# Kernel optimization log

Hardware: AMD Instinct MI355X
Metric: run time of the kernel (lower is better)

The kernel has to match this reference:

```python
import jax, jax.numpy as jnp
import numpy as np

D_MODEL, D_HIDDEN, N_EXPERTS, TOP_K = 1024, 2048, 8, 2


def setup_inputs() -> dict:
    key = jax.random.key(0)
    ks = jax.random.split(key, 8)
    s_in = 1.0 / np.sqrt(D_MODEL)
    s_hid = 1.0 / np.sqrt(D_HIDDEN)
    return {
        "x": jax.random.normal(ks[0], (1, 2048, D_MODEL), dtype=jnp.float32),
        # stacked expert weights, stored (in, out) so y = x @ W + b
        "W1": jax.random.normal(ks[1], (N_EXPERTS, D_MODEL, D_HIDDEN), dtype=jnp.float32) * s_in,
        "b1": jnp.zeros((N_EXPERTS, D_HIDDEN), dtype=jnp.float32),
        "W2": jax.random.normal(ks[2], (N_EXPERTS, D_MODEL, D_HIDDEN), dtype=jnp.float32) * s_in,
        "b2": jnp.zeros((N_EXPERTS, D_HIDDEN), dtype=jnp.float32),
        "Wo": jax.random.normal(ks[3], (N_EXPERTS, D_HIDDEN, D_MODEL), dtype=jnp.float32) * s_hid,
        "bo": jnp.zeros((N_EXPERTS, D_MODEL), dtype=jnp.float32),
        "Wr": jax.random.normal(ks[4], (D_MODEL, N_EXPERTS), dtype=jnp.float32) * s_in,
        "br": jnp.zeros((N_EXPERTS,), dtype=jnp.float32),
    }


def reference(x, W1, b1, W2, b2, Wo, bo, Wr, br):
    B, S, D = x.shape
    T = B * S
    xf = x.reshape(T, D)

    # router
    logits = xf @ Wr + br                      # [T, E]
    probs = jax.nn.softmax(logits, axis=-1)
    topk_probs, topk_idx = jax.lax.top_k(probs, TOP_K)  # [T, K]

    # combine weights: c[t, e] = sum_k topk_probs[t, k] * 1[topk_idx[t, k] == e]
    c = jnp.zeros((T, N_EXPERTS), dtype=xf.dtype)
    c = c.at[jnp.arange(T)[:, None], topk_idx].add(topk_probs)  # [T, E]

    # per-expert SwiGLU FFN applied densely, then masked-combined (same math
    # as the original gather/scatter loop since c[t,e]=0 for unrouted experts)
    h = jnp.einsum('td,edh->eth', xf, W1) + b1[:, None, :]   # [E, T, H]
    g = jnp.einsum('td,edh->eth', xf, W2) + b2[:, None, :]
    y = jnp.einsum('eth,ehd->etd', h * jax.nn.silu(g), Wo) + bo[:, None, :]
    out = jnp.einsum('etd,te->td', y, c).reshape(B, S, D)

    probs_mean = probs.mean(axis=0)
    lb_loss = (probs_mean * probs_mean).sum() * N_EXPERTS
    return out, lb_loss
```

## Files before the change

### kernel.cpp

```cpp
#include <hip/hip_runtime.h>
#include <hip/hip_bf16.h>

#define T_TOK 2048
#define DM 1024
#define DH 2048
#define NE 8
#define MT_MAX 40

using bf16x8 = __attribute__((ext_vector_type(8))) short;
using f32x4  = __attribute__((ext_vector_type(4))) float;

__device__ __forceinline__ unsigned short f2bf(float f) {
  union { float f; unsigned u; } v; v.f = f;
  unsigned r = v.u + 0x7FFFu + ((v.u >> 16) & 1u);
  return (unsigned short)(r >> 16);
}
__device__ __forceinline__ unsigned pk2(float a, float b) {
  return (unsigned)f2bf(a) | ((unsigned)f2bf(b) << 16);
}

#define GLOAD16(gsrc, ldst)                                                        \
  __builtin_amdgcn_global_load_lds(                                                \
      (const __attribute__((address_space(1))) unsigned int*)(gsrc),               \
      (__attribute__((address_space(3))) unsigned int*)(ldst), 16, 0, 0)

__global__ void k_init(int* __restrict__ cnt) {
  if (threadIdx.x < NE) cnt[threadIdx.x] = 0;
}

__global__ __launch_bounds__(256) void k_wconv(
    const float* __restrict__ x, const float* __restrict__ Wr, const float* __restrict__ br,
    int* __restrict__ cnt, int* __restrict__ idx, float* __restrict__ wgt,
    int* __restrict__ t2r, float* __restrict__ probs, unsigned short* __restrict__ xb,
    const float* __restrict__ W1, const float* __restrict__ W2, const float* __restrict__ Wo,
    unsigned short* __restrict__ W1T, unsigned short* __restrict__ W2T,
    unsigned short* __restrict__ WoT)
{
  __shared__ __align__(16) unsigned short tb[2][64*64];
  const int tid = threadIdx.x;

  if (blockIdx.x < 512) {
    const int wave = tid >> 6, l = tid & 63;
    const int tok = blockIdx.x * 4 + wave;
    float xv[16];
#pragma unroll
    for (int i = 0; i < 16; ++i) xv[i] = x[tok*DM + l + 64*i];
#pragma unroll
    for (int i = 0; i < 16; ++i) xb[tok*DM + l + 64*i] = f2bf(xv[i]);

    float acc[8] = {0.f,0.f,0.f,0.f,0.f,0.f,0.f,0.f};
#pragma unroll
    for (int i = 0; i < 16; ++i) {
      const float4* wp = (const float4*)&Wr[(size_t)(l + 64*i)*NE];
      float4 wa = wp[0], wb = wp[1];
      acc[0] += xv[i]*wa.x; acc[1] += xv[i]*wa.y; acc[2] += xv[i]*wa.z; acc[3] += xv[i]*wa.w;
      acc[4] += xv[i]*wb.x; acc[5] += xv[i]*wb.y; acc[6] += xv[i]*wb.z; acc[7] += xv[i]*wb.w;
    }
#pragma unroll
    for (int e = 0; e < 8; ++e) {
#pragma unroll
      for (int off = 32; off; off >>= 1) acc[e] += __shfl_xor(acc[e], off, 64);
      acc[e] += br[e];
    }
    float mx = acc[0];
#pragma unroll
    for (int e = 1; e < 8; ++e) mx = fmaxf(mx, acc[e]);
    float p[8], s = 0.f;
#pragma unroll
    for (int e = 0; e < 8; ++e) { p[e] = expf(acc[e] - mx); s += p[e]; }
    float inv = 1.f / s;
#pragma unroll
    for (int e = 0; e < 8; ++e) p[e] *= inv;

    int e0 = 0; float p0 = p[0];
#pragma unroll
    for (int e = 1; e < 8; ++e) if (p[e] > p0) { p0 = p[e]; e0 = e; }
    int e1 = -1; float p1 = -1.f;
#pragma unroll
    for (int e = 0; e < 8; ++e) { if (e == e0) continue; if (p[e] > p1) { p1 = p[e]; e1 = e; } }

    if (l == 0) {
#pragma unroll
      for (int e = 0; e < 8; ++e) probs[tok*NE + e] = p[e];
      int pos0 = atomicAdd(&cnt[e0], 1);
      idx[e0*T_TOK + pos0] = tok; wgt[e0*T_TOK + pos0] = p0;
      t2r[tok*2 + 0] = e0*T_TOK + pos0;
      int pos1 = atomicAdd(&cnt[e1], 1);
      idx[e1*T_TOK + pos1] = tok; wgt[e1*T_TOK + pos1] = p1;
      t2r[tok*2 + 1] = e1*T_TOK + pos1;
    }
    return;
  }

  const int bx = tid >> 4;
  const int by = tid & 15;
  const int rn = tid >> 3;
  const int sl8 = tid & 7;

#pragma unroll
  for (int it = 0; it < 4; ++it) {
    int tt = (blockIdx.x - 512) * 4 + it;
    const float* in; unsigned short* outT; int nCs;
    int R, C;
    if (tt < 4096)      { in = W1; outT = W1T; R = DM; C = DH; nCs = 5; }
    else if (tt < 8192) { in = W2; outT = W2T; R = DM; C = DH; nCs = 5; tt -= 4096; }
    else                { in = Wo; outT = WoT; R = DH; C = DM; nCs = 4; tt -= 8192; }
    const int e  = tt >> 9;
    const int te = tt & 511;
    const int r0 = (te >> nCs) << 6;
    const int c0 = (te & ((1 << nCs) - 1)) << 6;

    float4 v[4];
#pragma unroll
    for (int i = 0; i < 4; ++i)
      v[i] = *(const float4*)&in[((size_t)e*R + r0 + bx*4 + i)*C + c0 + by*4];

    unsigned short* B = tb[it & 1];
#pragma unroll
    for (int j = 0; j < 4; ++j) {
      int n = by*4 + j;
      uint2 w;
      w.x = pk2(((const float*)&v[0])[j], ((const float*)&v[1])[j]);
      w.y = pk2(((const float*)&v[2])[j], ((const float*)&v[3])[j]);
      int byteoff = n*128 + (((bx >> 1) ^ ((n >> 2) & 7)) * 16) + (bx & 1) * 8;
      *(uint2*)((char*)B + byteoff) = w;
    }
    __syncthreads();

#pragma unroll
    for (int h = 0; h < 2; ++h) {
      int n = rn + h*32;
      int byteoff = n*128 + ((sl8 ^ ((n >> 2) & 7)) * 16);
      uint4 w = *(const uint4*)((const char*)B + byteoff);
      *(uint4*)&outT[((size_t)e*C + c0 + n)*R + r0 + sl8*8] = w;
    }
  }
}

__global__ __launch_bounds__(256) void k_finalize(
    const int* __restrict__ cnt, int* __restrict__ rb,
    const float* __restrict__ probs, float* __restrict__ out,
    int* __restrict__ MTp, int* __restrict__ mtab)
{
  __shared__ float red[8][256];
  const int tid = threadIdx.x;
  float s[8] = {0.f,0.f,0.f,0.f,0.f,0.f,0.f,0.f};
  for (int t = tid; t < T_TOK; t += 256) {
#pragma unroll
    for (int e = 0; e < 8; ++e) s[e] += probs[t*NE + e];
  }
#pragma unroll
  for (int e = 0; e < 8; ++e) red[e][tid] = s[e];
  __syncthreads();
  for (int w = 128; w > 0; w >>= 1) {
    if (tid < w) {
#pragma unroll
      for (int e = 0; e < 8; ++e) red[e][tid] += red[e][tid + w];
    }
    __syncthreads();
  }
  if (tid == 0) {
    float lb = 0.f;
#pragma unroll
    for (int e = 0; e < 8; ++e) {
      float mean = red[e][0] * (1.f / T_TOK);
      lb += mean * mean;
    }
    out[2097152] = lb * NE;
    int r = 0, mc = 0;
#pragma unroll
    for (int e = 0; e < 8; ++e) {
      rb[e] = r; r += cnt[e];
      int nmt = (cnt[e] + 127) / 128;
      for (int j = 0; j < nmt; ++j) mtab[mc++] = (e << 16) | j;
    }
    *MTp = mc;
  }
}

#define TM1 128
#define TN1 64
#define BKK 64

__global__ __launch_bounds__(256) void k_ffn1b(
    const unsigned short* __restrict__ xb,
    const unsigned short* __restrict__ W1T, const float* __restrict__ b1,
    const unsigned short* __restrict__ W2T, const float* __restrict__ b2,
    const int* __restrict__ cnt, const int* __restrict__ rbp,
    const int* __restrict__ idx, unsigned short* __restrict__ act,
    const int* __restrict__ MTp, const int* __restrict__ mtab)
{
  const int mtg = blockIdx.y;
  if (mtg >= *MTp) return;
  const int code = mtab[mtg];
  const int e = code >> 16, mt = code & 0xffff;
  const int Me = cnt[e];
  const int m0 = mt * TM1;
  const int nt = blockIdx.x;
  const int n0 = nt * TN1;

  __shared__ __align__(16) unsigned short As[TM1*BKK];
  __shared__ __align__(16) unsigned short Bh[TN1*BKK];
  __shared__ __align__(16) unsigned short Bg[TN1*BKK];
  __shared__ int toks[TM1];

  const int tid = threadIdx.x;
  if (tid < TM1) toks[tid] = idx[e*T_TOK + min(m0 + tid, Me - 1)];
  __syncthreads();

  const int lane = tid & 63;
  const int wave = tid >> 6;
  const int wm = wave >> 1, wn = wave & 1;
  const int row16 = lane & 15, kg = lane >> 4;
  const int sl = lane & 7;
  const int lr = lane >> 3;

  const unsigned short* asrc[4];
#pragma unroll
  for (int i = 0; i < 4; ++i) {
    int r = (wave*4 + i)*8 + lr;
    asrc[i] = &xb[(size_t)toks[r]*DM + ((sl ^ (r & 7)) * 8)];
  }
  const unsigned short *bsrc1[2], *bsrc2[2];
#pragma unroll
  for (int j = 0; j < 2; ++j) {
    int r = (wave*2 + j)*8 + lr;
    size_t gb = ((size_t)e*DH + n0 + r)*DM + ((sl ^ (r & 7)) * 8);
    bsrc1[j] = &W1T[gb]; bsrc2[j] = &W2T[gb];
  }

  f32x4 ah[4][2], ag[4][2];
#pragma unroll
  for (int i = 0; i < 4; ++i)
#pragma unroll
    for (int j = 0; j < 2; ++j) { ah[i][j] = 0.f; ag[i][j] = 0.f; }

  for (int k0 = 0; k0 < DM; k0 += BKK) {
#pragma unroll
    for (int i = 0; i < 4; ++i)
      GLOAD16(asrc[i] + k0, &As[(wave*4 + i)*512]);
#pragma unroll
    for (int j = 0; j < 2; ++j) {
      GLOAD16(bsrc1[j] + k0, &Bh[(wave*2 + j)*512]);
      GLOAD16(bsrc2[j] + k0, &Bg[(wave*2 + j)*512]);
    }
    __syncthreads();
#pragma unroll
    for (int ks = 0; ks < 2; ++ks) {
      const int kslot = ks*4 + kg;
      bf16x8 a[4], vbh[2], vbg[2];
#pragma unroll
      for (int mi = 0; mi < 4; ++mi) {
        int m = wm*64 + mi*16 + row16;
        a[mi] = *(const bf16x8*)&As[m*BKK + ((kslot ^ (m & 7)) * 8)];
      }
#pragma unroll
      for (int ni = 0; ni < 2; ++ni) {
        int n = wn*32 + ni*16 + row16;
        int off = n*BKK + ((kslot ^ (n & 7)) * 8);
        vbh[ni] = *(const bf16x8*)&Bh[off];
        vbg[ni] = *(const bf16x8*)&Bg[off];
      }
#pragma unroll
      for (int mi = 0; mi < 4; ++mi)
#pragma unroll
        for (int ni = 0; ni < 2; ++ni) {
          ah[mi][ni] = __builtin_amdgcn_mfma_f32_16x16x32_bf16(a[mi], vbh[ni], ah[mi][ni], 0, 0, 0);
          ag[mi][ni] = __builtin_amdgcn_mfma_f32_16x16x32_bf16(a[mi], vbg[ni], ag[mi][ni], 0, 0, 0);
        }
    }
    __syncthreads();
  }

  const int rb = rbp[e];
#pragma unroll
  for (int mi = 0; mi < 4; ++mi) {
#pragma unroll
    for (int i = 0; i < 4; ++i) {
      int rloc = wm*64 + mi*16 + (lane >> 4)*4 + i;
      int m = m0 + rloc;
      if (m < Me) {
#pragma unroll
        for (int ni = 0; ni < 2; ++ni) {
          int col = n0 + wn*32 + ni*16 + row16;
          float h = ah[mi][ni][i] + b1[e*DH + col];
          float g = ag[mi][ni][i] + b2[e*DH + col];
          float sg = g / (1.f + __expf(-g));
          act[(size_t)(rb + m)*DH + col] = f2bf(h * sg);
        }
      }
    }
  }
}

__global__ __launch_bounds__(256) void k_ffn2b(
    const unsigned short* __restrict__ act,
    const unsigned short* __restrict__ WoT, const float* __restrict__ bo,
    const int* __restrict__ cnt, const int* __restrict__ rbp,
    float* __restrict__ ys,
    const int* __restrict__ MTp, const int* __restrict__ mtab)
{
  const int mtg = blockIdx.y;
  if (mtg >= *MTp) return;
  const int code = mtab[mtg];
  const int e = code >> 16, mt = code & 0xffff;
  const int Me = cnt[e];
  const int m0 = mt * TM1;
  const int nt = blockIdx.x;
  const int n0 = nt * TN1;
  const int rb = rbp[e];

  __shared__ __align__(16) unsigned short As[TM1*BKK];
  __shared__ __align__(16) unsigned short Bs[TN1*BKK];

  const int tid = threadIdx.x;
  const int lane = tid & 63;
  const int wave = tid >> 6;
  const int wm = wave >> 1, wn = wave & 1;
  const int row16 = lane & 15, kg = lane >> 4;
  const int sl = lane & 7;
  const int lr = lane >> 3;

  const unsigned short* asrc[4];
#pragma unroll
  for (int i = 0; i < 4; ++i) {
    int r = (wave*4 + i)*8 + lr;
    int grow = rb + min(m0 + r, Me - 1);
    asrc[i] = &act[(size_t)grow*DH + ((sl ^ (r & 7)) * 8)];
  }
  const unsigned short* bsrc[2];
#pragma unroll
  for (int j = 0; j < 2; ++j) {
    int r = (wave*2 + j)*8 + lr;
    bsrc[j] = &WoT[((size_t)e*DM + n0 + r)*DH + ((sl ^ (r & 7)) * 8)];
  }

  f32x4 acc[4][2];
#pragma unroll
  for (int i = 0; i < 4; ++i)
#pragma unroll
    for (int j = 0; j < 2; ++j) acc[i][j] = 0.f;

  for (int k0 = 0; k0 < DH; k0 += BKK) {
#pragma unroll
    for (int i = 0; i < 4; ++i)
      GLOAD16(asrc[i] + k0, &As[(wave*4 + i)*512]);
#pragma unroll
    for (int j = 0; j < 2; ++j)
      GLOAD16(bsrc[j] + k0, &Bs[(wave*2 + j)*512]);
    __syncthreads();
#pragma unroll
    for (int ks = 0; ks < 2; ++ks) {
      const int kslot = ks*4 + kg;
      bf16x8 a[4], b[2];
#pragma unroll
      for (int mi = 0; mi < 4; ++mi) {
        int m = wm*64 + mi*16 + row16;
        a[mi] = *(const bf16x8*)&As[m*BKK + ((kslot ^ (m & 7)) * 8)];
      }
#pragma unroll
      for (int ni = 0; ni < 2; ++ni) {
        int n = wn*32 + ni*16 + row16;
        b[ni] = *(const bf16x8*)&Bs[n*BKK + ((kslot ^ (n & 7)) * 8)];
      }
#pragma unroll
      for (int mi = 0; mi < 4; ++mi)
#pragma unroll
        for (int ni = 0; ni < 2; ++ni)
          acc[mi][ni] = __builtin_amdgcn_mfma_f32_16x16x32_bf16(a[mi], b[ni], acc[mi][ni], 0, 0, 0);
    }
    __syncthreads();
  }

#pragma unroll
  for (int mi = 0; mi < 4; ++mi) {
#pragma unroll
    for (int i = 0; i < 4; ++i) {
      int rloc = wm*64 + mi*16 + (lane >> 4)*4 + i;
      int m = m0 + rloc;
      if (m < Me) {
#pragma unroll
        for (int ni = 0; ni < 2; ++ni) {
          int col = n0 + wn*32 + ni*16 + row16;
          ys[(size_t)(rb + m)*DM + col] = acc[mi][ni][i] + bo[e*DM + col];
        }
      }
    }
  }
}

__global__ __launch_bounds__(256) void k_combine(
    const float* __restrict__ ys, const int* __restrict__ t2r,
    const int* __restrict__ rbp, const float* __restrict__ wgt,
    float* __restrict__ out)
{
  const int t = blockIdx.x, tid = threadIdx.x;
  const int c0 = t2r[t*2 + 0], c1 = t2r[t*2 + 1];
  const float w0 = wgt[c0], w1 = wgt[c1];
  const int r0 = rbp[c0 >> 11] + (c0 & 2047);
  const int r1 = rbp[c1 >> 11] + (c1 & 2047);
  const float4* p0 = (const float4*)&ys[(size_t)r0*DM];
  const float4* p1 = (const float4*)&ys[(size_t)r1*DM];
  float4* po = (float4*)&out[(size_t)t*DM];
  float4 a = p0[tid], b = p1[tid];
  float4 r;
  r.x = w0*a.x + w1*b.x; r.y = w0*a.y + w1*b.y;
  r.z = w0*a.z + w1*b.z; r.w = w0*a.w + w1*b.w;
  po[tid] = r;
}

extern "C" void kernel_launch(void* const* d_in, const int* in_sizes, int n_in,
                              void* d_out, int out_size, void* d_ws, size_t ws_size,
                              hipStream_t stream)
{
  const float* x  = (const float*)d_in[0];
  const float* W1 = (const float*)d_in[1];
  const float* b1 = (const float*)d_in[2];
  const float* W2 = (const float*)d_in[3];
  const float* b2 = (const float*)d_in[4];
  const float* Wo = (const float*)d_in[5];
  const float* bo = (const float*)d_in[6];
  const float* Wr = (const float*)d_in[7];
  const float* br = (const float*)d_in[8];
  float* out = (float*)d_out;

  char* ws = (char*)d_ws;
  int*   cnt   = (int*)(ws + 0);
  int*   rb    = (int*)(ws + 64);
  int*   MTp   = (int*)(ws + 128);
  int*   mtab  = (int*)(ws + 192);
  int*   t2r   = (int*)(ws + 4096);
  int*   idx   = (int*)(ws + 32*1024);
  float* wgt   = (float*)(ws + 96*1024);
  float* probs = (float*)(ws + 160*1024);
  unsigned short* xb  = (unsigned short*)(ws + 256*1024);
  unsigned short* act = (unsigned short*)(ws + 5ull*1024*1024);
  float* ysb = (float*)(ws + 21ull*1024*1024);
  unsigned short* W1T = (unsigned short*)(ws + 40ull*1024*1024);
  unsigned short* W2T = (unsigned short*)(ws + 72ull*1024*1024);
  unsigned short* WoT = (unsigned short*)(ws + 104ull*1024*1024);

  k_init<<<1, 64, 0, stream>>>(cnt);
  k_wconv<<<512 + 3072, 256, 0, stream>>>(x, Wr, br, cnt, idx, wgt, t2r, probs, xb,
                                          W1, W2, Wo, W1T, W2T, WoT);
  k_finalize<<<1, 256, 0, stream>>>(cnt, rb, probs, out, MTp, mtab);
  k_ffn1b<<<dim3(DH/TN1, MT_MAX), 256, 0, stream>>>(xb, W1T, b1, W2T, b2, cnt, rb, idx, act, MTp, mtab);
  k_ffn2b<<<dim3(DM/TN1, MT_MAX), 256, 0, stream>>>(act, WoT, bo, cnt, rb, ysb, MTp, mtab);
  k_combine<<<T_TOK, 256, 0, stream>>>(ysb, t2r, rb, wgt, out);
}
```

Baseline: 219.4 us.

## Store transposed bf16 weights in contiguous 256x64 tiles for streaming writes

The weight conversion kernel now has each block handle one 64-row by 256-column tile in a single pass. It writes the bf16 result as a contiguous 32KB chunk, replacing the strided transposed rows. The GEMM kernels change their B-operand addressing to read this tiled layout, stepping through K-chunks with a fixed stride. The aim is fully coalesced, sequential stores in the conversion, which happens inside the timed region, and more contiguous weight reads in the GEMMs. In exchange the block uses a larger LDS buffer, and the chunk pointer line contains an odd comma expression that happens to evaluate correctly.

```diff
diff --git a/kernel.cpp b/kernel.cpp
--- a/kernel.cpp
+++ b/kernel.cpp
@@ -36,7 +36,7 @@
     unsigned short* __restrict__ W1T, unsigned short* __restrict__ W2T,
     unsigned short* __restrict__ WoT)
 {
-  __shared__ __align__(16) unsigned short tb[2][64*64];
+  __shared__ __align__(16) unsigned short tb[256*64];
   const int tid = threadIdx.x;
 
   if (blockIdx.x < 512) {
@@ -92,48 +92,46 @@
     return;
   }
 
-  const int bx = tid >> 4;
-  const int by = tid & 15;
-  const int rn = tid >> 3;
-  const int sl8 = tid & 7;
-
-#pragma unroll
-  for (int it = 0; it < 4; ++it) {
-    int tt = (blockIdx.x - 512) * 4 + it;
-    const float* in; unsigned short* outT; int nCs;
-    int R, C;
-    if (tt < 4096)      { in = W1; outT = W1T; R = DM; C = DH; nCs = 5; }
-    else if (tt < 8192) { in = W2; outT = W2T; R = DM; C = DH; nCs = 5; tt -= 4096; }
-    else                { in = Wo; outT = WoT; R = DH; C = DM; nCs = 4; tt -= 8192; }
-    const int e  = tt >> 9;
-    const int te = tt & 511;
-    const int r0 = (te >> nCs) << 6;
-    const int c0 = (te & ((1 << nCs) - 1)) << 6;
-
+  int tt = blockIdx.x - 512;
+  const float* in; unsigned short* outT; int R, C, nTb;
+  if (tt < 1024)      { in = W1; outT = W1T; R = DM; C = DH; nTb = 3; }
+  else if (tt < 2048) { in = W2; outT = W2T; R = DM; C = DH; nTb = 3; tt -= 1024; }
+  else                { in = Wo; outT = WoT; R = DH; C = DM; nTb = 2; tt -= 2048; }
+  const int e  = tt >> 7;
+  const int te = tt & 127;
+  const int r0 = (te >> nTb) * 64;
+  const int c0 = (te & ((1 << nTb) - 1)) * 256;
+
+  const int nq = tid & 63;
+  const int kqb = tid >> 6;
+
+#pragma unroll
+  for (int p = 0; p < 4; ++p) {
+    const int kq = p*4 + kqb;
     float4 v[4];
 #pragma unroll
     for (int i = 0; i < 4; ++i)
-      v[i] = *(const float4*)&in[((size_t)e*R + r0 + bx*4 + i)*C + c0 + by*4];
-
-    unsigned short* B = tb[it & 1];
+      v[i] = *(const float4*)&in[((size_t)e*R + r0 + kq*4 + i)*C + c0 + nq*4];
 #pragma unroll
     for (int j = 0; j < 4; ++j) {
-      int n = by*4 + j;
+      const int n = nq*4 + j;
       uint2 w;
       w.x = pk2(((const float*)&v[0])[j], ((const float*)&v[1])[j]);
       w.y = pk2(((const float*)&v[2])[j], ((const float*)&v[3])[j]);
-      int byteoff = n*128 + (((bx >> 1) ^ ((n >> 2) & 7)) * 16) + (bx & 1) * 8;
-      *(uint2*)((char*)B + byteoff) = w;
-    }
-    __syncthreads();
-
-#pragma unroll
-    for (int h = 0; h < 2; ++h) {
-      int n = rn + h*32;
-      int byteoff = n*128 + ((sl8 ^ ((n >> 2) & 7)) * 16);
-      uint4 w = *(const uint4*)((const char*)B + byteoff);
-      *(uint4*)&outT[((size_t)e*C + c0 + n)*R + r0 + sl8*8] = w;
-    }
+      const int slot8 = kq ^ ((nq & 7) << 1);
+      *(uint2*)((char*)tb + n*128 + slot8*8) = w;
+    }
+  }
+  __syncthreads();
+
+  unsigned short* chunk = outT + (size_t)(blockIdx.x >= 2560 + 512 - 3072 + 3072 ? 0 : 0, (size_t)( ( (e << 7) | te ) ) * 16384);
+#pragma unroll
+  for (int p2 = 0; p2 < 8; ++p2) {
+    const int u = p2*256 + tid;
+    const int n = u >> 3, k16 = u & 7;
+    const int slot16 = k16 ^ ((n >> 2) & 7);
+    uint4 w = *(const uint4*)((const char*)tb + n*128 + slot16*16);
+    *(uint4*)&chunk[(size_t)u * 8] = w;
   }
 }
 
@@ -222,10 +220,11 @@
     asrc[i] = &xb[(size_t)toks[r]*DM + ((sl ^ (r & 7)) * 8)];
   }
   const unsigned short *bsrc1[2], *bsrc2[2];
+  const int nt256 = n0 >> 8, nsub = n0 & 255;
 #pragma unroll
   for (int j = 0; j < 2; ++j) {
     int r = (wave*2 + j)*8 + lr;
-    size_t gb = ((size_t)e*DH + n0 + r)*DM + ((sl ^ (r & 7)) * 8);
+    size_t gb = ((size_t)e*128 + nt256)*16384 + (size_t)(nsub + r)*64 + ((sl ^ (r & 7)) * 8);
     bsrc1[j] = &W1T[gb]; bsrc2[j] = &W2T[gb];
   }
 
@@ -236,13 +235,14 @@
     for (int j = 0; j < 2; ++j) { ah[i][j] = 0.f; ag[i][j] = 0.f; }
 
   for (int k0 = 0; k0 < DM; k0 += BKK) {
+    const size_t bko = (size_t)k0 * 2048;
 #pragma unroll
     for (int i = 0; i < 4; ++i)
       GLOAD16(asrc[i] + k0, &As[(wave*4 + i)*512]);
 #pragma unroll
     for (int j = 0; j < 2; ++j) {
-      GLOAD16(bsrc1[j] + k0, &Bh[(wave*2 + j)*512]);
-      GLOAD16(bsrc2[j] + k0, &Bg[(wave*2 + j)*512]);
+      GLOAD16(bsrc1[j] + bko, &Bh[(wave*2 + j)*512]);
+      GLOAD16(bsrc2[j] + bko, &Bg[(wave*2 + j)*512]);
     }
     __syncthreads();
 #pragma unroll
@@ -329,10 +329,12 @@
     asrc[i] = &act[(size_t)grow*DH + ((sl ^ (r & 7)) * 8)];
   }
   const unsigned short* bsrc[2];
+  const int nt256 = n0 >> 8, nsub = n0 & 255;
 #pragma unroll
   for (int j = 0; j < 2; ++j) {
     int r = (wave*2 + j)*8 + lr;
-    bsrc[j] = &WoT[((size_t)e*DM + n0 + r)*DH + ((sl ^ (r & 7)) * 8)];
+    size_t gb = ((size_t)e*128 + nt256)*16384 + (size_t)(nsub + r)*64 + ((sl ^ (r & 7)) * 8);
+    bsrc[j] = &WoT[gb];
   }
 
   f32x4 acc[4][2];
@@ -342,12 +344,13 @@
     for (int j = 0; j < 2; ++j) acc[i][j] = 0.f;
 
   for (int k0 = 0; k0 < DH; k0 += BKK) {
+    const size_t bko = (size_t)k0 * 1024;
 #pragma unroll
     for (int i = 0; i < 4; ++i)
       GLOAD16(asrc[i] + k0, &As[(wave*4 + i)*512]);
 #pragma unroll
     for (int j = 0; j < 2; ++j)
-      GLOAD16(bsrc[j] + k0, &Bs[(wave*2 + j)*512]);
+      GLOAD16(bsrc[j] + bko, &Bs[(wave*2 + j)*512]);
     __syncthreads();
 #pragma unroll
     for (int ks = 0; ks < 2; ++ks) {
```

Result: faster. 206.4 us (-5.9%).
